# Performance work log

Hardware: AMD Instinct MI355X
Metric: run time of the kernel (lower is better)

The kernel has to match this reference:

```python
import jax, jax.numpy as jnp
import numpy as np

B, T, S, D, H = 16, 2048, 2048, 1024, 24  # batch, text len, encoded len, feature dim, head dim


def setup_inputs() -> dict:
    key = jax.random.key(0)
    ks = jax.random.split(key, 6)
    return {
        "encoded": jax.random.normal(ks[0], (B, S, D), dtype=jnp.float32),
        "text": jax.random.normal(ks[1], (B, T, D), dtype=jnp.float32),
        "wq": jax.random.normal(ks[2], (D, H), dtype=jnp.float32) * 0.02,
        "wk": jax.random.normal(ks[3], (D, H), dtype=jnp.float32) * 0.02,
        "wv": jax.random.normal(ks[4], (D, H), dtype=jnp.float32) * 0.02,
        "wh": jax.random.normal(ks[5], (H, D), dtype=jnp.float32) * 0.02,
    }


def reference(encoded, text, wq, wk, wv, wh):
    q = text @ wq          # [B, T, H]
    k = encoded @ wk       # [B, S, H]
    v = encoded @ wv       # [B, S, H]
    a = jnp.einsum("bth,bsh->bts", q, k)   # [B, T, S]
    # NOTE: original applies softmax over dim=1 (the QUERY axis), not the key axis.
    a = jax.nn.softmax(a, axis=1)
    h1 = jnp.einsum("bts,bsh->bth", a, v)  # [B, T, H]
    return h1 @ wh         # [B, T, D]
```

## Files before the change

### kernel.cpp

```cpp
#include <hip/hip_runtime.h>
#include <hip/hip_bf16.h>

#define B_ 16
#define T_ 2048
#define S_ 2048
#define D_ 1024
#define H_ 24
#define NROW_ (B_ * T_)
#define BS_ (B_ * S_)
#define QN32_ ((size_t)NROW_ * 32)

typedef float f32x16 __attribute__((ext_vector_type(16)));
typedef __bf16 bf16x8 __attribute__((ext_vector_type(8)));

union B8u { int4 i; bf16x8 b; };
__device__ inline bf16x8 pun(int4 v) { B8u u; u.i = v; return u.b; }

__device__ inline ushort f2bf(float f) {
  uint u = __float_as_uint(f);
  u += 0x7fffu + ((u >> 16) & 1u);
  return (ushort)(u >> 16);
}
__device__ inline float bf2f(ushort u) { return __uint_as_float(((uint)u) << 16); }

__device__ inline f32x16 mfma32(bf16x8 a, bf16x8 b, f32x16 c) {
  return __builtin_amdgcn_mfma_f32_32x32x16_bf16(a, b, c, 0, 0, 0);
}

__device__ inline uint cvtpk(float a, float b) {
  uint r;
  asm("v_cvt_pk_bf16_f32 %0, %1, %2" : "=v"(r) : "v"(a), "v"(b));
  return r;
}

__global__ __launch_bounds__(256) void prep_w(
    const float* __restrict__ wq, const float* __restrict__ wk,
    const float* __restrict__ wv, ushort* __restrict__ wpk) {
  int i = blockIdx.x * 256 + threadIdx.x;
  if (i >= 3 * 128 * H_) return;
  int which = i / (128 * H_);
  int rem = i - which * 128 * H_;
  int k8g = rem / H_, n = rem - k8g * H_;
  const float* w = (which == 0) ? wq : (which == 1) ? wk : wv;
  ushort t[8];
#pragma unroll
  for (int j = 0; j < 8; ++j) t[j] = f2bf(w[(k8g * 8 + j) * H_ + n]);
  *(int4*)&wpk[(size_t)i * 8] = *(const int4*)t;
}

__global__ __launch_bounds__(256) void proj_unified(
    const float* __restrict__ text, const float* __restrict__ encoded,
    const ushort* __restrict__ wpk, ushort* __restrict__ qb,
    ushort* __restrict__ kbuf, float* __restrict__ vv) {
  __shared__ __align__(16) ushort sA[4][8][32][8];
  __shared__ __align__(16) float sRed[4][1088];

  const int tid = threadIdx.x;
  const int lane = tid & 63, lo = lane & 31, hi = lane >> 5, w = tid >> 6;
  const bool kvmode = (blockIdx.x >= 1024);
  const int bid = kvmode ? (blockIdx.x - 1024) : blockIdx.x;
  const float* in = kvmode ? encoded : text;
  const ushort* wp1 = wpk + (size_t)(kvmode ? 1 : 0) * 128 * H_ * 8;
  const ushort* wp2 = wpk + (size_t)2 * 128 * H_ * 8;
  const long rowbase = (long)bid * 32;
  const int ne = (lo < H_) ? lo : 0;

  const float* base = in + rowbase * D_ + w * 256;

  f32x16 acc = {};
  f32x16 acc2 = {};

#pragma unroll
  for (int win = 0; win < 4; ++win) {
    float4 fv[8];
#pragma unroll
    for (int i = 0; i < 8; ++i) {
      int g = lane + 64 * i, row = g >> 4, f4 = g & 15;
      fv[i] = *(const float4*)(base + row * D_ + win * 64 + f4 * 4);
    }
#pragma unroll
    for (int i = 0; i < 8; ++i) {
      int g = lane + 64 * i, row = g >> 4, f4 = g & 15;
      int k8 = f4 >> 1, par = f4 & 1;
      uint p0 = cvtpk(fv[i].x, fv[i].y), p1 = cvtpk(fv[i].z, fv[i].w);
      *(uint2*)&sA[w][k8][row ^ k8][par * 4] = make_uint2(p0, p1);
    }
#pragma unroll
    for (int cl = 0; cl < 4; ++cl) {
      const int k8 = 2 * cl + hi;
      bf16x8 a = pun(*(const int4*)&sA[w][k8][lo ^ k8][0]);
      const int k8g = w * 32 + win * 8 + k8;
      bf16x8 b1 = pun(*(const int4*)&wp1[(size_t)(k8g * H_ + ne) * 8]);
      acc = mfma32(a, b1, acc);
      if (kvmode) {
        bf16x8 b2 = pun(*(const int4*)&wp2[(size_t)(k8g * H_ + ne) * 8]);
        acc2 = mfma32(a, b2, acc2);
      }
    }
  }

#pragma unroll
  for (int r = 0; r < 16; ++r) sRed[w][lane * 17 + r] = acc[r];
  __syncthreads();
  {
    const int qd = tid >> 6, l = tid & 63, lo2 = l & 31, hi2 = l >> 5;
    ushort* o1 = (kvmode ? kbuf : qb);
#pragma unroll
    for (int rr = 0; rr < 4; ++rr) {
      const int r = qd * 4 + rr;
      float s = sRed[0][l * 17 + r] + sRed[1][l * 17 + r] +
                sRed[2][l * 17 + r] + sRed[3][l * 17 + r];
      const int mrow = rr + 8 * qd + 4 * hi2;
      o1[(size_t)(rowbase + mrow) * 32 + lo2] = (lo2 < H_) ? f2bf(s) : (ushort)0;
    }
  }
  if (kvmode) {
    __syncthreads();
#pragma unroll
    for (int r = 0; r < 16; ++r) sRed[w][lane * 17 + r] = acc2[r];
    __syncthreads();
    const int qd = tid >> 6, l = tid & 63, lo2 = l & 31, hi2 = l >> 5;
    if (lo2 < H_) {
#pragma unroll
      for (int rr = 0; rr < 4; ++rr) {
        const int r = qd * 4 + rr;
        float s = sRed[0][l * 17 + r] + sRed[1][l * 17 + r] +
                  sRed[2][l * 17 + r] + sRed[3][l * 17 + r];
        const int mrow = rr + 8 * qd + 4 * hi2;
        vv[(size_t)(rowbase + mrow) * H_ + lo2] = s;
      }
    }
  }
}

__global__ __launch_bounds__(256) void colsum_mfma(
    const ushort* __restrict__ qb, const ushort* __restrict__ kb,
    float* __restrict__ dpart) {
  __shared__ __align__(16) ushort sQ[4 * 32 * 8];
  const int tid = threadIdx.x;
  const int lane = tid & 63;
  const int lo = lane & 31, hi = lane >> 5;
  const int w = tid >> 6;
  const int b = blockIdx.y;
  const int s0 = blockIdx.x * 128 + w * 32;
  const int tpart = blockIdx.z;

  const ushort* krow = kb + ((size_t)b * S_ + s0 + lo) * 32;
  bf16x8 k0 = pun(*(const int4*)(krow + hi * 8));
  bf16x8 k1 = pun(*(const int4*)(krow + 16 + hi * 8));

  float dl = 0.f;
  for (int tc = 0; tc < 16; ++tc) {
    const int tbase = tpart * 512 + tc * 32;
    if (tid < 128) {
      int t = tid >> 2, j = tid & 3;
      *(int4*)&sQ[j * 256 + t * 8] =
          *(const int4*)(qb + ((size_t)b * T_ + tbase + t) * 32 + j * 8);
    }
    __syncthreads();
    bf16x8 qa = pun(*(const int4*)&sQ[hi * 256 + lo * 8]);
    bf16x8 qc = pun(*(const int4*)&sQ[(2 + hi) * 256 + lo * 8]);
    f32x16 c = {};
    c = mfma32(qa, k0, c);
    c = mfma32(qc, k1, c);
#pragma unroll
    for (int r = 0; r < 16; ++r) dl += __expf(c[r]);
    __syncthreads();
  }
  dl += __shfl_xor(dl, 32);
  if (hi == 0) dpart[(size_t)tpart * BS_ + (size_t)b * S_ + s0 + lo] = dl;
}

__global__ __launch_bounds__(256) void vscale_kernel(
    const float* __restrict__ vv, const float* __restrict__ dpart,
    ushort* __restrict__ vsT) {
  int gid = blockIdx.x * 256 + threadIdx.x;
  int s4 = gid & 511;
  int h = (gid >> 9) & 31;
  int b = gid >> 14;
  int s0 = s4 * 4;
  ushort4 ov;
  if (h < H_) {
    const float* vp = vv + ((size_t)b * S_ + s0) * H_ + h;
    const float* dp = dpart + (size_t)b * S_ + s0;
    float dv[4];
#pragma unroll
    for (int i = 0; i < 4; ++i) {
      float d = dp[i] + dp[BS_ + i] + dp[2 * BS_ + i] + dp[3 * BS_ + i];
      dv[i] = 1.0f / d;
    }
    ov.x = f2bf(vp[0 * H_] * dv[0]);
    ov.y = f2bf(vp[1 * H_] * dv[1]);
    ov.z = f2bf(vp[2 * H_] * dv[2]);
    ov.w = f2bf(vp[3 * H_] * dv[3]);
  } else {
    ov.x = ov.y = ov.z = ov.w = 0;
  }
  *(ushort4*)&vsT[((size_t)b * 32 + h) * S_ + s0] = ov;
}

__global__ __launch_bounds__(256) void attn_mfma(
    const ushort* __restrict__ qb, const ushort* __restrict__ kb,
    const ushort* __restrict__ vsT, ushort* __restrict__ h1p) {
  __shared__ __align__(16) ushort sK[4 * 32 * 8];
  __shared__ __align__(16) ushort sV[4 * 32 * 8];
  const int tid = threadIdx.x;
  const int lane = tid & 63;
  const int lo = lane & 31, hi = lane >> 5;
  const int w = tid >> 6;
  const int b = blockIdx.y;
  const int t0 = blockIdx.x * 128 + w * 32;
  const int spart = blockIdx.z;

  const ushort* qrow = qb + ((size_t)b * T_ + t0 + lo) * 32;
  bf16x8 q0 = pun(*(const int4*)(qrow + hi * 8));
  bf16x8 q1 = pun(*(const int4*)(qrow + 16 + hi * 8));

  f32x16 hacc = {};
  for (int sc = 0; sc < 16; ++sc) {
    const int sbase = spart * 512 + sc * 32;
    if (tid < 128) {
      int s = tid >> 2, j = tid & 3;
      *(int4*)&sK[j * 256 + s * 8] =
          *(const int4*)(kb + ((size_t)b * S_ + sbase + s) * 32 + j * 8);
    } else {
      int i2 = tid - 128;
      int h = i2 >> 2, q = i2 & 3;
      *(int4*)&sV[q * 256 + h * 8] =
          *(const int4*)(vsT + ((size_t)b * 32 + h) * S_ + sbase + q * 8);
    }
    __syncthreads();
    bf16x8 ka = pun(*(const int4*)&sK[hi * 256 + lo * 8]);
    bf16x8 kc = pun(*(const int4*)&sK[(2 + hi) * 256 + lo * 8]);
    bf16x8 va = pun(*(const int4*)&sV[hi * 256 + lo * 8]);
    bf16x8 vc = pun(*(const int4*)&sV[(2 + hi) * 256 + lo * 8]);
    f32x16 c = {};
    c = mfma32(ka, q0, c);
    c = mfma32(kc, q1, c);
    uint pk[8];
#pragma unroll
    for (int m = 0; m < 8; ++m) {
      float plo = __expf(c[2 * m]);
      float phi = __expf(c[2 * m + 1]);
      pk[m] = cvtpk(plo, phi);
    }
    asm("v_permlane32_swap_b32 %0, %1" : "+v"(pk[0]), "+v"(pk[2]));
    asm("v_permlane32_swap_b32 %0, %1" : "+v"(pk[1]), "+v"(pk[3]));
    asm("v_permlane32_swap_b32 %0, %1" : "+v"(pk[4]), "+v"(pk[6]));
    asm("v_permlane32_swap_b32 %0, %1" : "+v"(pk[5]), "+v"(pk[7]));
    int4 f0 = make_int4(pk[0], pk[1], pk[2], pk[3]);
    int4 f1 = make_int4(pk[4], pk[5], pk[6], pk[7]);
    hacc = mfma32(pun(f0), va, hacc);
    hacc = mfma32(pun(f1), vc, hacc);
    __syncthreads();
  }
  ushort* o = h1p + (size_t)spart * QN32_ + (size_t)b * T_ * 32;
#pragma unroll
  for (int r = 0; r < 16; ++r) {
    int trow = t0 + (r & 3) + 8 * (r >> 2) + 4 * hi;
    o[(size_t)trow * 32 + lo] = f2bf(hacc[r]);
  }
}

__global__ __launch_bounds__(256) void out_kernel(const ushort* __restrict__ h1p,
                                                  const float* __restrict__ wh,
                                                  float* __restrict__ out) {
  __shared__ __align__(16) float s_h1[16 * 24];
  const int tid = threadIdx.x;
  const long rbase = (long)blockIdx.x * 16;
  if (tid < 48) {
    const int r = tid / 3, c8 = tid - 3 * r;
    float s[8] = {0.f, 0.f, 0.f, 0.f, 0.f, 0.f, 0.f, 0.f};
#pragma unroll
    for (int part = 0; part < 4; ++part) {
      int4 v = *(const int4*)&h1p[(size_t)part * QN32_ +
                                  (size_t)(rbase + r) * 32 + c8 * 8];
      const ushort* u = (const ushort*)&v;
#pragma unroll
      for (int j = 0; j < 8; ++j) s[j] += bf2f(u[j]);
    }
#pragma unroll
    for (int j = 0; j < 8; ++j) s_h1[r * 24 + c8 * 8 + j] = s[j];
  }
  __syncthreads();
  for (int c = 0; c < 4; ++c) {
    const int dd = c * 256 + tid;
    float wr[24];
#pragma unroll
    for (int h = 0; h < 24; ++h) wr[h] = wh[h * D_ + dd];
#pragma unroll 1
    for (int r = 0; r < 16; ++r) {
      float a = 0.f;
#pragma unroll
      for (int j = 0; j < 6; ++j) {
        float4 hv = *(const float4*)(s_h1 + r * 24 + 4 * j);
        a = fmaf(hv.x, wr[4 * j], a);
        a = fmaf(hv.y, wr[4 * j + 1], a);
        a = fmaf(hv.z, wr[4 * j + 2], a);
        a = fmaf(hv.w, wr[4 * j + 3], a);
      }
      out[(rbase + r) * D_ + dd] = a;
    }
  }
}

extern "C" void kernel_launch(void* const* d_in, const int* in_sizes, int n_in,
                              void* d_out, int out_size, void* d_ws,
                              size_t ws_size, hipStream_t stream) {
  const float* encoded = (const float*)d_in[0];
  const float* text = (const float*)d_in[1];
  const float* wq = (const float*)d_in[2];
  const float* wk = (const float*)d_in[3];
  const float* wv = (const float*)d_in[4];
  const float* wh = (const float*)d_in[5];
  float* out = (float*)d_out;

  ushort* qb = (ushort*)d_ws;
  ushort* kbuf = qb + QN32_;
  float* vv = (float*)(kbuf + QN32_);
  float* dpart = vv + (size_t)BS_ * H_;
  ushort* vsT = (ushort*)(dpart + 4 * BS_);
  ushort* h1p = vsT + (size_t)B_ * 32 * S_;
  ushort* wpk = h1p + 4 * QN32_;

  prep_w<<<36, 256, 0, stream>>>(wq, wk, wv, wpk);
  proj_unified<<<2048, 256, 0, stream>>>(text, encoded, wpk, qb, kbuf, vv);
  colsum_mfma<<<dim3(S_ / 128, B_, 4), 256, 0, stream>>>(qb, kbuf, dpart);
  vscale_kernel<<<(B_ * 32 * (S_ / 4)) / 256, 256, 0, stream>>>(vv, dpart, vsT);
  attn_mfma<<<dim3(T_ / 128, B_, 4), 256, 0, stream>>>(qb, kbuf, vsT, h1p);
  out_kernel<<<NROW_ / 16, 256, 0, stream>>>(h1p, wh, out);
}
```

Baseline: 161.6 us.

## Double-buffer projection input via direct global-to-LDS loads with swizzle

The projection kernel now streams fp32 input tiles straight into shared memory with global_load_lds, double-buffered across the four K windows and gated by explicit vmcnt waits. Conversion to bf16 moves to after the LDS read. Weight fragments are preloaded into registers up front, and launch bounds request two blocks per CU. This is meant to overlap HBM loads with MFMA work and drop the register round-trip, at the cost of a larger fp32 LDS footprint (64KB per block) and more register pressure.

```diff
diff --git a/kernel.cpp b/kernel.cpp
--- a/kernel.cpp
+++ b/kernel.cpp
@@ -32,6 +32,9 @@
   asm("v_cvt_pk_bf16_f32 %0, %1, %2" : "=v"(r) : "v"(a), "v"(b));
   return r;
 }
+
+#define AS1C(p) ((const __attribute__((address_space(1))) void*)((const void*)(p)))
+#define AS3(p) ((__attribute__((address_space(3))) void*)((void*)(p)))
 
 __global__ __launch_bounds__(256) void prep_w(
     const float* __restrict__ wq, const float* __restrict__ wk,
@@ -48,12 +51,11 @@
   *(int4*)&wpk[(size_t)i * 8] = *(const int4*)t;
 }
 
-__global__ __launch_bounds__(256) void proj_unified(
+__global__ __launch_bounds__(256, 2) void proj_unified(
     const float* __restrict__ text, const float* __restrict__ encoded,
     const ushort* __restrict__ wpk, ushort* __restrict__ qb,
     ushort* __restrict__ kbuf, float* __restrict__ vv) {
-  __shared__ __align__(16) ushort sA[4][8][32][8];
-  __shared__ __align__(16) float sRed[4][1088];
+  __shared__ __align__(16) float sA[4][2][2048];
 
   const int tid = threadIdx.x;
   const int lane = tid & 63, lo = lane & 31, hi = lane >> 5, w = tid >> 6;
@@ -65,42 +67,69 @@
   const long rowbase = (long)bid * 32;
   const int ne = (lo < H_) ? lo : 0;
 
-  const float* base = in + rowbase * D_ + w * 256;
+  int4 bfr1[16], bfr2[16];
+#pragma unroll
+  for (int win = 0; win < 4; ++win) {
+#pragma unroll
+    for (int cl = 0; cl < 4; ++cl) {
+      const int k8g = w * 32 + win * 8 + 2 * cl + hi;
+      bfr1[win * 4 + cl] = *(const int4*)&wp1[(size_t)(k8g * H_ + ne) * 8];
+      if (kvmode)
+        bfr2[win * 4 + cl] = *(const int4*)&wp2[(size_t)(k8g * H_ + ne) * 8];
+    }
+  }
+
+  const int srow = lane >> 4;
+  const int c16l = lane & 15;
+  const float* gbase = in + rowbase * D_ + w * 256;
 
   f32x16 acc = {};
   f32x16 acc2 = {};
 
+#define STAGE(win_, buf_)                                                     \
+  {                                                                           \
+    _Pragma("unroll") for (int i = 0; i < 8; ++i) {                           \
+      const int row = i * 4 + srow;                                           \
+      const int c16s = c16l ^ ((row & 7) << 1);      \
+      const float* g = gbase + (size_t)row * D_ + (win_)*64 + c16s * 4;       \
+      __builtin_amdgcn_global_load_lds(AS1C(g), AS3(&sA[w][buf_][i * 256]),   \
+                                       16, 0, 0);                             \
+    }                                                                         \
+  }
+
+  STAGE(0, 0);
 #pragma unroll
   for (int win = 0; win < 4; ++win) {
-    float4 fv[8];
-#pragma unroll
-    for (int i = 0; i < 8; ++i) {
-      int g = lane + 64 * i, row = g >> 4, f4 = g & 15;
-      fv[i] = *(const float4*)(base + row * D_ + win * 64 + f4 * 4);
-    }
-#pragma unroll
-    for (int i = 0; i < 8; ++i) {
-      int g = lane + 64 * i, row = g >> 4, f4 = g & 15;
-      int k8 = f4 >> 1, par = f4 & 1;
-      uint p0 = cvtpk(fv[i].x, fv[i].y), p1 = cvtpk(fv[i].z, fv[i].w);
-      *(uint2*)&sA[w][k8][row ^ k8][par * 4] = make_uint2(p0, p1);
-    }
+    const int buf = win & 1;
+    __builtin_amdgcn_sched_barrier(0);
+    if (win < 3) {
+      if (win == 0) STAGE(1, 1);
+      if (win == 1) STAGE(2, 0);
+      if (win == 2) STAGE(3, 1);
+      asm volatile("s_waitcnt vmcnt(8)" ::: "memory");
+    } else {
+      asm volatile("s_waitcnt vmcnt(0)" ::: "memory");
+    }
+    __builtin_amdgcn_sched_barrier(0);
 #pragma unroll
     for (int cl = 0; cl < 4; ++cl) {
       const int k8 = 2 * cl + hi;
-      bf16x8 a = pun(*(const int4*)&sA[w][k8][lo ^ k8][0]);
-      const int k8g = w * 32 + win * 8 + k8;
-      bf16x8 b1 = pun(*(const int4*)&wp1[(size_t)(k8g * H_ + ne) * 8]);
-      acc = mfma32(a, b1, acc);
-      if (kvmode) {
-        bf16x8 b2 = pun(*(const int4*)&wp2[(size_t)(k8g * H_ + ne) * 8]);
-        acc2 = mfma32(a, b2, acc2);
-      }
-    }
-  }
-
-#pragma unroll
-  for (int r = 0; r < 16; ++r) sRed[w][lane * 17 + r] = acc[r];
+      const int c16 = (2 * k8) ^ ((lo & 7) << 1);
+      float4 ga = *(const float4*)&sA[w][buf][lo * 64 + c16 * 4];
+      float4 gb = *(const float4*)&sA[w][buf][lo * 64 + c16 * 4 + 4];
+      uint p0 = cvtpk(ga.x, ga.y), p1 = cvtpk(ga.z, ga.w);
+      uint p2 = cvtpk(gb.x, gb.y), p3 = cvtpk(gb.z, gb.w);
+      bf16x8 a = pun(make_int4(p0, p1, p2, p3));
+      acc = mfma32(a, pun(bfr1[win * 4 + cl]), acc);
+      if (kvmode) acc2 = mfma32(a, pun(bfr2[win * 4 + cl]), acc2);
+    }
+  }
+#undef STAGE
+
+  float* sR = (float*)sA;
+  __syncthreads();
+#pragma unroll
+  for (int r = 0; r < 16; ++r) sR[w * 1088 + lane * 17 + r] = acc[r];
   __syncthreads();
   {
     const int qd = tid >> 6, l = tid & 63, lo2 = l & 31, hi2 = l >> 5;
@@ -108,8 +137,8 @@
 #pragma unroll
     for (int rr = 0; rr < 4; ++rr) {
       const int r = qd * 4 + rr;
-      float s = sRed[0][l * 17 + r] + sRed[1][l * 17 + r] +
-                sRed[2][l * 17 + r] + sRed[3][l * 17 + r];
+      float s = sR[0 * 1088 + l * 17 + r] + sR[1 * 1088 + l * 17 + r] +
+                sR[2 * 1088 + l * 17 + r] + sR[3 * 1088 + l * 17 + r];
       const int mrow = rr + 8 * qd + 4 * hi2;
       o1[(size_t)(rowbase + mrow) * 32 + lo2] = (lo2 < H_) ? f2bf(s) : (ushort)0;
     }
@@ -117,15 +146,15 @@
   if (kvmode) {
     __syncthreads();
 #pragma unroll
-    for (int r = 0; r < 16; ++r) sRed[w][lane * 17 + r] = acc2[r];
+    for (int r = 0; r < 16; ++r) sR[w * 1088 + lane * 17 + r] = acc2[r];
     __syncthreads();
     const int qd = tid >> 6, l = tid & 63, lo2 = l & 31, hi2 = l >> 5;
     if (lo2 < H_) {
 #pragma unroll
       for (int rr = 0; rr < 4; ++rr) {
         const int r = qd * 4 + rr;
-        float s = sRed[0][l * 17 + r] + sRed[1][l * 17 + r] +
-                  sRed[2][l * 17 + r] + sRed[3][l * 17 + r];
+        float s = sR[0 * 1088 + l * 17 + r] + sR[1 * 1088 + l * 17 + r] +
+                  sR[2 * 1088 + l * 17 + r] + sR[3 * 1088 + l * 17 + r];
         const int mrow = rr + 8 * qd + 4 * hi2;
         vv[(size_t)(rowbase + mrow) * H_ + lo2] = s;
       }
```

Result: faster. 156.5 us (-3.1%).

## Split projection into Q and KV kernels with full-row staging and preloaded weights

Applied to the files above, without the earlier changes.

Replaces the unified projection kernel with two specialized kernels, removing the per-block kvmode branching. Each warp now loads its whole 256-column slice of 32 rows into LDS up front, with double-buffered register groups and an XOR swizzle, instead of four small windows. Weight fragments are preloaded into registers before the MFMA loop. This aims to raise memory-level parallelism on the bandwidth-bound fp32 input read, at the cost of larger LDS (64KB) and more registers, which limits occupancy to 2 blocks per CU, plus an extra kernel launch.

```diff
diff --git a/kernel.cpp b/kernel.cpp
--- a/kernel.cpp
+++ b/kernel.cpp
@@ -48,90 +48,140 @@
   *(int4*)&wpk[(size_t)i * 8] = *(const int4*)t;
 }
 
-__global__ __launch_bounds__(256) void proj_unified(
-    const float* __restrict__ text, const float* __restrict__ encoded,
-    const ushort* __restrict__ wpk, ushort* __restrict__ qb,
+
+#define LOADG(dst, g)                                                        \
+  _Pragma("unroll") for (int j = 0; j < 8; ++j) dst[j] =                     \
+      *(const float4*)(rowp + (size_t)((g) * 8 + j) * D_ + l * 4);
+#define WRITEG(src, g)                                                       \
+  _Pragma("unroll") for (int j = 0; j < 8; ++j) {                            \
+    const int row = (g) * 8 + j;                                             \
+    uint p0 = cvtpk(src[j].x, src[j].y), p1 = cvtpk(src[j].z, src[j].w);     \
+    const int s = (l >> 1) ^ (row & 7);                                      \
+    *(uint2*)&sA[w][row][s * 8 + (l & 1) * 4] = make_uint2(p0, p1);          \
+  }
+
+__global__ __launch_bounds__(256, 2) void proj_q(
+    const float* __restrict__ in, const ushort* __restrict__ wpk,
+    ushort* __restrict__ qb) {
+  __shared__ __align__(16) ushort sA[4][32][256];
+
+  const int tid = threadIdx.x;
+  const int lane = tid & 63, lo = lane & 31, hi = lane >> 5, w = tid >> 6;
+  const int l = lane;
+  const long rowbase = (long)blockIdx.x * 32;
+  const int ne = (lo < H_) ? lo : 0;
+  const float* rowp = in + rowbase * D_ + w * 256;
+
+  float4 ga[8], gb[8];
+  LOADG(ga, 0); LOADG(gb, 1);
+  WRITEG(ga, 0); LOADG(ga, 2);
+  WRITEG(gb, 1); LOADG(gb, 3);
+  WRITEG(ga, 2); WRITEG(gb, 3);
+
+  int4 bfr[16];
+#pragma unroll
+  for (int c = 0; c < 16; ++c) {
+    const int k8g = w * 32 + 2 * c + hi;
+    bfr[c] = *(const int4*)&wpk[(size_t)(k8g * H_ + ne) * 8];
+  }
+  f32x16 acc = {};
+#pragma unroll
+  for (int c = 0; c < 16; ++c) {
+    const int s = (2 * c + hi) ^ (lo & 7);
+    bf16x8 a = pun(*(const int4*)&sA[w][lo][s * 8]);
+    acc = mfma32(a, pun(bfr[c]), acc);
+  }
+
+  float* sR = (float*)sA;
+  __syncthreads();
+#pragma unroll
+  for (int r = 0; r < 16; ++r) sR[w * 1088 + lane * 17 + r] = acc[r];
+  __syncthreads();
+  const int qd = tid >> 6, l2 = tid & 63, lo2 = l2 & 31, hi2 = l2 >> 5;
+#pragma unroll
+  for (int rr = 0; rr < 4; ++rr) {
+    const int r = qd * 4 + rr;
+    float s = sR[0 * 1088 + l2 * 17 + r] + sR[1 * 1088 + l2 * 17 + r] +
+              sR[2 * 1088 + l2 * 17 + r] + sR[3 * 1088 + l2 * 17 + r];
+    const int mrow = rr + 8 * qd + 4 * hi2;
+    qb[(size_t)(rowbase + mrow) * 32 + lo2] = (lo2 < H_) ? f2bf(s) : (ushort)0;
+  }
+}
+
+__global__ __launch_bounds__(256, 2) void proj_kv(
+    const float* __restrict__ in, const ushort* __restrict__ wpk,
     ushort* __restrict__ kbuf, float* __restrict__ vv) {
-  __shared__ __align__(16) ushort sA[4][8][32][8];
-  __shared__ __align__(16) float sRed[4][1088];
+  __shared__ __align__(16) ushort sA[4][32][256];
 
   const int tid = threadIdx.x;
   const int lane = tid & 63, lo = lane & 31, hi = lane >> 5, w = tid >> 6;
-  const bool kvmode = (blockIdx.x >= 1024);
-  const int bid = kvmode ? (blockIdx.x - 1024) : blockIdx.x;
-  const float* in = kvmode ? encoded : text;
-  const ushort* wp1 = wpk + (size_t)(kvmode ? 1 : 0) * 128 * H_ * 8;
+  const int l = lane;
+  const long rowbase = (long)blockIdx.x * 32;
+  const int ne = (lo < H_) ? lo : 0;
+  const float* rowp = in + rowbase * D_ + w * 256;
+  const ushort* wp1 = wpk + (size_t)1 * 128 * H_ * 8;
   const ushort* wp2 = wpk + (size_t)2 * 128 * H_ * 8;
-  const long rowbase = (long)bid * 32;
-  const int ne = (lo < H_) ? lo : 0;
-
-  const float* base = in + rowbase * D_ + w * 256;
-
+
+  float4 ga[8], gb[8];
+  LOADG(ga, 0); LOADG(gb, 1);
+  WRITEG(ga, 0); LOADG(ga, 2);
+  WRITEG(gb, 1); LOADG(gb, 3);
+  WRITEG(ga, 2); WRITEG(gb, 3);
+
+  int4 bfr1[16], bfr2[16];
+#pragma unroll
+  for (int c = 0; c < 16; ++c) {
+    const int k8g = w * 32 + 2 * c + hi;
+    bfr1[c] = *(const int4*)&wp1[(size_t)(k8g * H_ + ne) * 8];
+    bfr2[c] = *(const int4*)&wp2[(size_t)(k8g * H_ + ne) * 8];
+  }
   f32x16 acc = {};
   f32x16 acc2 = {};
-
-#pragma unroll
-  for (int win = 0; win < 4; ++win) {
-    float4 fv[8];
-#pragma unroll
-    for (int i = 0; i < 8; ++i) {
-      int g = lane + 64 * i, row = g >> 4, f4 = g & 15;
-      fv[i] = *(const float4*)(base + row * D_ + win * 64 + f4 * 4);
-    }
-#pragma unroll
-    for (int i = 0; i < 8; ++i) {
-      int g = lane + 64 * i, row = g >> 4, f4 = g & 15;
-      int k8 = f4 >> 1, par = f4 & 1;
-      uint p0 = cvtpk(fv[i].x, fv[i].y), p1 = cvtpk(fv[i].z, fv[i].w);
-      *(uint2*)&sA[w][k8][row ^ k8][par * 4] = make_uint2(p0, p1);
-    }
-#pragma unroll
-    for (int cl = 0; cl < 4; ++cl) {
-      const int k8 = 2 * cl + hi;
-      bf16x8 a = pun(*(const int4*)&sA[w][k8][lo ^ k8][0]);
-      const int k8g = w * 32 + win * 8 + k8;
-      bf16x8 b1 = pun(*(const int4*)&wp1[(size_t)(k8g * H_ + ne) * 8]);
-      acc = mfma32(a, b1, acc);
-      if (kvmode) {
-        bf16x8 b2 = pun(*(const int4*)&wp2[(size_t)(k8g * H_ + ne) * 8]);
-        acc2 = mfma32(a, b2, acc2);
-      }
-    }
-  }
-
-#pragma unroll
-  for (int r = 0; r < 16; ++r) sRed[w][lane * 17 + r] = acc[r];
+#pragma unroll
+  for (int c = 0; c < 16; ++c) {
+    const int s = (2 * c + hi) ^ (lo & 7);
+    bf16x8 a = pun(*(const int4*)&sA[w][lo][s * 8]);
+    acc = mfma32(a, pun(bfr1[c]), acc);
+    acc2 = mfma32(a, pun(bfr2[c]), acc2);
+  }
+
+  float* sR = (float*)sA;
+  __syncthreads();
+#pragma unroll
+  for (int r = 0; r < 16; ++r) sR[w * 1088 + lane * 17 + r] = acc[r];
   __syncthreads();
   {
-    const int qd = tid >> 6, l = tid & 63, lo2 = l & 31, hi2 = l >> 5;
-    ushort* o1 = (kvmode ? kbuf : qb);
+    const int qd = tid >> 6, l2 = tid & 63, lo2 = l2 & 31, hi2 = l2 >> 5;
 #pragma unroll
     for (int rr = 0; rr < 4; ++rr) {
       const int r = qd * 4 + rr;
-      float s = sRed[0][l * 17 + r] + sRed[1][l * 17 + r] +
-                sRed[2][l * 17 + r] + sRed[3][l * 17 + r];
+      float s = sR[0 * 1088 + l2 * 17 + r] + sR[1 * 1088 + l2 * 17 + r] +
+                sR[2 * 1088 + l2 * 17 + r] + sR[3 * 1088 + l2 * 17 + r];
       const int mrow = rr + 8 * qd + 4 * hi2;
-      o1[(size_t)(rowbase + mrow) * 32 + lo2] = (lo2 < H_) ? f2bf(s) : (ushort)0;
-    }
-  }
-  if (kvmode) {
-    __syncthreads();
-#pragma unroll
-    for (int r = 0; r < 16; ++r) sRed[w][lane * 17 + r] = acc2[r];
-    __syncthreads();
-    const int qd = tid >> 6, l = tid & 63, lo2 = l & 31, hi2 = l >> 5;
+      kbuf[(size_t)(rowbase + mrow) * 32 + lo2] =
+          (lo2 < H_) ? f2bf(s) : (ushort)0;
+    }
+  }
+  __syncthreads();
+#pragma unroll
+  for (int r = 0; r < 16; ++r) sR[w * 1088 + lane * 17 + r] = acc2[r];
+  __syncthreads();
+  {
+    const int qd = tid >> 6, l2 = tid & 63, lo2 = l2 & 31, hi2 = l2 >> 5;
     if (lo2 < H_) {
 #pragma unroll
       for (int rr = 0; rr < 4; ++rr) {
         const int r = qd * 4 + rr;
-        float s = sRed[0][l * 17 + r] + sRed[1][l * 17 + r] +
-                  sRed[2][l * 17 + r] + sRed[3][l * 17 + r];
+        float s = sR[0 * 1088 + l2 * 17 + r] + sR[1 * 1088 + l2 * 17 + r] +
+                  sR[2 * 1088 + l2 * 17 + r] + sR[3 * 1088 + l2 * 17 + r];
         const int mrow = rr + 8 * qd + 4 * hi2;
         vv[(size_t)(rowbase + mrow) * H_ + lo2] = s;
       }
     }
   }
 }
+#undef LOADG
+#undef WRITEG
 
 __global__ __launch_bounds__(256) void colsum_mfma(
     const ushort* __restrict__ qb, const ushort* __restrict__ kb,
@@ -324,7 +374,8 @@
   ushort* wpk = h1p + 4 * QN32_;
 
   prep_w<<<36, 256, 0, stream>>>(wq, wk, wv, wpk);
-  proj_unified<<<2048, 256, 0, stream>>>(text, encoded, wpk, qb, kbuf, vv);
+  proj_q<<<1024, 256, 0, stream>>>(text, wpk, qb);
+  proj_kv<<<1024, 256, 0, stream>>>(encoded, wpk, kbuf, vv);
   colsum_mfma<<<dim3(S_ / 128, B_, 4), 256, 0, stream>>>(qb, kbuf, dpart);
   vscale_kernel<<<(B_ * 32 * (S_ / 4)) / 256, 256, 0, stream>>>(vv, dpart, vsT);
   attn_mfma<<<dim3(T_ / 128, B_, 4), 256, 0, stream>>>(qb, kbuf, vsT, h1p);
```

After: 164.2 us. Within noise of the previous version (+1.6%).
